# Kernel tuning notes

Hardware: AMD Instinct MI355X
Metric: run time of the kernel (lower is better)

Reference implementation:

```python
import jax, jax.numpy as jnp
import numpy as np

EMBED_DIM = 256
SEQ_LEN = 4096
BATCH = 8
ALPHA = 0.99


def setup_inputs() -> dict:
    key = jax.random.key(0)
    k_x, k_w, k_b = jax.random.split(key, 3)
    x = jax.random.normal(k_x, (BATCH, SEQ_LEN, EMBED_DIM), dtype=jnp.float32)
    # nn.Linear(embed_dim, 3*embed_dim): store as [d, 3d] so y = x @ Wqkv + bqkv
    Wqkv = jax.random.normal(k_w, (EMBED_DIM, 3 * EMBED_DIM), dtype=jnp.float32) * (EMBED_DIM ** -0.5)
    bqkv = jax.random.normal(k_b, (3 * EMBED_DIM,), dtype=jnp.float32) * 0.02
    return {"x": x, "Wqkv": Wqkv, "bqkv": bqkv}


def reference(x, Wqkv, bqkv):
    bs, sl, d = x.shape
    qkv = x @ Wqkv + bqkv                      # [bs, sl, 3d]
    q, k, v = jnp.split(qkv, 3, axis=-1)       # each [bs, sl, d]
    # causal * exponential-decay mask: M[i, j] = alpha**(i-j) for j <= i else 0
    i = jnp.arange(sl, dtype=jnp.float32)
    M = jnp.where(i[:, None] >= i[None, :],
                  jnp.power(jnp.float32(ALPHA), i[:, None] - i[None, :]),
                  0.0)                          # [sl, sl]
    scores = jnp.einsum('bqd,bkd->bqk', q, k) / jnp.sqrt(jnp.float32(d))
    out = jnp.einsum('bqk,bkd->bqd', scores * M, v)
    return out
```

## Files before the change

### kernel.cpp

```cpp
#include <hip/hip_runtime.h>

typedef __bf16 bf16x8 __attribute__((ext_vector_type(8)));
typedef float f32x4 __attribute__((ext_vector_type(4)));
typedef unsigned short u16;
typedef unsigned int u32;
typedef u16 u16x4 __attribute__((ext_vector_type(4)));

#define L2ALPHA (-0.014499569f)

static __device__ __forceinline__ u16 f2bf(float f) {
    u32 u = __builtin_bit_cast(u32, f);
    return (u16)((u + 0x7FFFu + ((u >> 16) & 1u)) >> 16);
}

static __device__ __forceinline__ void gl2lds16(const void* g, void* l) {
    __builtin_amdgcn_global_load_lds(
        (const __attribute__((address_space(1))) u32*)g,
        (__attribute__((address_space(3))) u32*)l, 16, 0, 0);
}

__global__ __launch_bounds__(256, 2) void proj_kernel(
        const float* __restrict__ x, const float* __restrict__ Wq,
        const float* __restrict__ bias,
        u16* __restrict__ qb, u16* __restrict__ kb, u16* __restrict__ vb)
{
    __shared__ __align__(16) u16 Bs[32 * 128 * 8];
    __shared__ __align__(16) u16 As[4 * 128 * 8];

    const int tid = threadIdx.x, lane = tid & 63, w = tid >> 6;
    const int l = blockIdx.x;
    const int nb = l >> 6;
    const int chunk = ((l >> 3) & 7) * 8 + (l & 7);
    const int n0 = nb * 128;
    const int wr = (w & 1) * 64, wc = (w >> 1) * 64;
    const int m = lane & 15, quad = lane >> 4;

    {
        const int col = tid & 127;
        const int khalf = tid >> 7;
        #pragma unroll
        for (int s = 0; s < 32; ++s) {
            int k0 = (khalf + 2 * s) * 4;
            u16x4 h;
            #pragma unroll
            for (int i = 0; i < 4; ++i)
                h[i] = f2bf(Wq[(k0 + i) * 768 + n0 + col]);
            *(u16x4*)&Bs[((k0 >> 3) * 128 + col) * 8 + (k0 & 7)] = h;
        }
    }

    for (int it = 0; it < 4; ++it) {
        const int m0 = (chunk * 4 + it) * 128;

        f32x4 acc[4][4];
        #pragma unroll
        for (int rt = 0; rt < 4; ++rt)
            #pragma unroll
            for (int ct = 0; ct < 4; ++ct)
                acc[rt][ct] = f32x4{0.f, 0.f, 0.f, 0.f};

        for (int kt = 0; kt < 8; ++kt) {
            __syncthreads();
            #pragma unroll
            for (int s = 0; s < 4; ++s) {
                int c = tid + 256 * s;
                int row = c >> 3, part = c & 7;
                const float4 v4 = *(const float4*)(x + (size_t)(m0 + row) * 256 + kt * 32 + part * 4);
                u16x4 h;
                h[0] = f2bf(v4.x); h[1] = f2bf(v4.y); h[2] = f2bf(v4.z); h[3] = f2bf(v4.w);
                *(u16x4*)&As[((part >> 1) * 128 + row) * 8 + (part & 1) * 4] = h;
            }
            __syncthreads();

            bf16x8 af[4], bfr[4];
            #pragma unroll
            for (int rt = 0; rt < 4; ++rt)
                af[rt] = *(const bf16x8*)&As[(quad * 128 + wr + rt * 16 + m) * 8];
            #pragma unroll
            for (int ct = 0; ct < 4; ++ct)
                bfr[ct] = *(const bf16x8*)&Bs[((kt * 4 + quad) * 128 + wc + ct * 16 + m) * 8];
            #pragma unroll
            for (int rt = 0; rt < 4; ++rt)
                #pragma unroll
                for (int ct = 0; ct < 4; ++ct)
                    acc[rt][ct] = __builtin_amdgcn_mfma_f32_16x16x32_bf16(
                        af[rt], bfr[ct], acc[rt][ct], 0, 0, 0);
        }

        const int b = m0 >> 12;
        const int jbase = (m0 & 4095) + wr;
        const int d0 = (nb & 1) * 128;

        if (nb < 2) {
            #pragma unroll
            for (int rt = 0; rt < 4; ++rt)
                #pragma unroll
                for (int ct = 0; ct < 4; ++ct) {
                    int coll = wc + ct * 16 + m;
                    float bv = bias[d0 + coll];
                    #pragma unroll
                    for (int r = 0; r < 4; ++r) {
                        int row = m0 + wr + rt * 16 + quad * 4 + r;
                        qb[(size_t)row * 256 + d0 + coll] = f2bf((acc[rt][ct][r] + bv) * 0.0625f);
                    }
                }
        } else if (nb < 4) {
            #pragma unroll
            for (int rt = 0; rt < 4; ++rt)
                #pragma unroll
                for (int ct = 0; ct < 4; ++ct) {
                    int d = d0 + wc + ct * 16 + m;
                    float bv = bias[256 + d];
                    int k8 = d >> 5, qk = (d >> 3) & 3, e = d & 7;
                    #pragma unroll
                    for (int r = 0; r < 4; ++r) {
                        int j = jbase + rt * 16 + quad * 4 + r;
                        int jt = j >> 5, hh = (j >> 4) & 1, mk = j & 15;
                        kb[((((size_t)(b * 128 + jt) * 2 + hh) * 8 + k8) * 64 + qk * 16 + mk) * 8 + e]
                            = f2bf(acc[rt][ct][r] + bv);
                    }
                }
        } else {
            #pragma unroll
            for (int rt = 0; rt < 4; ++rt)
                #pragma unroll
                for (int ct = 0; ct < 4; ++ct) {
                    int d = d0 + wc + ct * 16 + m;
                    float bv = bias[512 + d];
                    int dt = d >> 4, mv = d & 15;
                    int j = jbase + rt * 16 + quad * 4;
                    int jt = j >> 5, qv = (j >> 3) & 3, e0 = j & 7;
                    u16x4 hv;
                    #pragma unroll
                    for (int r = 0; r < 4; ++r) hv[r] = f2bf(acc[rt][ct][r] + bv);
                    *(u16x4*)&vb[(((size_t)(b * 128 + jt) * 16 + dt) * 64 + qv * 16 + mv) * 8 + e0] = hv;
                }
        }
    }
}

__global__ __launch_bounds__(256, 1) void attn_kernel(
        const u16* __restrict__ qb, const u16* __restrict__ kb,
        const u16* __restrict__ vb, float* __restrict__ out)
{
    __shared__ __align__(16) u16 Kf[2][8192];
    __shared__ __align__(16) u16 Vf[2][8192];
    __shared__ __align__(16) u16 Ps[4 * 2 * 16 * 40];

    const int tid = threadIdx.x, lane = tid & 63, w = tid >> 6;
    const int l = blockIdx.x;
    const int b = l & 7;
    const int m0 = (l >> 3) * 128;
    const int qrow0 = m0 + w * 32;
    const int m = lane & 15, quad = lane >> 4;
    const size_t rowbase = (size_t)b * 4096;

    bf16x8 qf[2][8];
    #pragma unroll
    for (int rg = 0; rg < 2; ++rg)
        #pragma unroll
        for (int k8 = 0; k8 < 8; ++k8)
            qf[rg][k8] = *(const bf16x8*)(qb + (rowbase + qrow0 + rg * 16 + m) * 256 + k8 * 32 + quad * 8);

    f32x4 acc[2][16];
    #pragma unroll
    for (int rg = 0; rg < 2; ++rg)
        #pragma unroll
        for (int dt = 0; dt < 16; ++dt)
            acc[rg][dt] = f32x4{0.f, 0.f, 0.f, 0.f};

    int t0 = (m0 - 1024) >> 5; if (t0 < 0) t0 = 0;
    const int t1 = (m0 >> 5) + 3;

    {
        const u16* kp = kb + (size_t)(b * 128 + t0) * 8192;
        const u16* vp = vb + (size_t)(b * 128 + t0) * 8192;
        #pragma unroll
        for (int s = 0; s < 4; ++s) {
            int c = tid + 256 * s;
            gl2lds16(kp + (size_t)c * 8, &Kf[0][c * 8]);
            gl2lds16(vp + (size_t)c * 8, &Vf[0][c * 8]);
        }
    }

    int p = 0;
    for (int t = t0; t <= t1; ++t) {
        __syncthreads();
        if (t < t1) {
            const u16* kp = kb + (size_t)(b * 128 + t + 1) * 8192;
            const u16* vp = vb + (size_t)(b * 128 + t + 1) * 8192;
            #pragma unroll
            for (int s = 0; s < 4; ++s) {
                int c = tid + 256 * s;
                gl2lds16(kp + (size_t)c * 8, &Kf[p ^ 1][c * 8]);
                gl2lds16(vp + (size_t)c * 8, &Vf[p ^ 1][c * 8]);
            }
        }
        const int j0 = t * 32;

        f32x4 s00{0.f,0.f,0.f,0.f}, s01{0.f,0.f,0.f,0.f};
        f32x4 s10{0.f,0.f,0.f,0.f}, s11{0.f,0.f,0.f,0.f};
        #pragma unroll
        for (int k8 = 0; k8 < 8; ++k8) {
            bf16x8 bf0 = *(const bf16x8*)&Kf[p][(k8 * 64 + lane) * 8];
            s00 = __builtin_amdgcn_mfma_f32_16x16x32_bf16(qf[0][k8], bf0, s00, 0, 0, 0);
            s01 = __builtin_amdgcn_mfma_f32_16x16x32_bf16(qf[1][k8], bf0, s01, 0, 0, 0);
        }
        #pragma unroll
        for (int k8 = 0; k8 < 8; ++k8) {
            bf16x8 bf1 = *(const bf16x8*)&Kf[p][((8 + k8) * 64 + lane) * 8];
            s10 = __builtin_amdgcn_mfma_f32_16x16x32_bf16(qf[0][k8], bf1, s10, 0, 0, 0);
            s11 = __builtin_amdgcn_mfma_f32_16x16x32_bf16(qf[1][k8], bf1, s11, 0, 0, 0);
        }

        #pragma unroll
        for (int rg = 0; rg < 2; ++rg) {
            f32x4 sh0 = rg ? s01 : s00;
            f32x4 sh1 = rg ? s11 : s10;
            #pragma unroll
            for (int r = 0; r < 4; ++r) {
                int i = qrow0 + rg * 16 + quad * 4 + r;
                int dd0 = i - (j0 + m);
                int dd1 = dd0 - 16;
                float w0 = (dd0 >= 0) ? __builtin_amdgcn_exp2f((float)dd0 * L2ALPHA) : 0.0f;
                float w1 = (dd1 >= 0) ? __builtin_amdgcn_exp2f((float)dd1 * L2ALPHA) : 0.0f;
                int rowb = ((w * 2 + rg) * 16 + quad * 4 + r) * 40;
                Ps[rowb + m]      = f2bf(sh0[r] * w0);
                Ps[rowb + 16 + m] = f2bf(sh1[r] * w1);
            }
        }
        asm volatile("s_waitcnt lgkmcnt(0)" ::: "memory");

        bf16x8 pa0 = *(const bf16x8*)&Ps[((w * 2 + 0) * 16 + m) * 40 + quad * 8];
        bf16x8 pa1 = *(const bf16x8*)&Ps[((w * 2 + 1) * 16 + m) * 40 + quad * 8];

        #pragma unroll
        for (int dt = 0; dt < 16; ++dt) {
            bf16x8 vf = *(const bf16x8*)&Vf[p][(dt * 64 + lane) * 8];
            acc[0][dt] = __builtin_amdgcn_mfma_f32_16x16x32_bf16(pa0, vf, acc[0][dt], 0, 0, 0);
            acc[1][dt] = __builtin_amdgcn_mfma_f32_16x16x32_bf16(pa1, vf, acc[1][dt], 0, 0, 0);
        }
        p ^= 1;
    }

    #pragma unroll
    for (int rg = 0; rg < 2; ++rg)
        #pragma unroll
        for (int dt = 0; dt < 16; ++dt)
            #pragma unroll
            for (int r = 0; r < 4; ++r)
                out[(rowbase + qrow0 + rg * 16 + quad * 4 + r) * 256 + dt * 16 + m] = acc[rg][dt][r];
}

extern "C" void kernel_launch(void* const* d_in, const int* in_sizes, int n_in,
                              void* d_out, int out_size, void* d_ws, size_t ws_size,
                              hipStream_t stream) {
    (void)in_sizes; (void)n_in; (void)out_size; (void)ws_size;
    const float* x    = (const float*)d_in[0];
    const float* Wq   = (const float*)d_in[1];
    const float* bias = (const float*)d_in[2];
    float* outp = (float*)d_out;

    const size_t per = (size_t)8 * 4096 * 256;
    u16* qb = (u16*)d_ws;
    u16* kb = qb + per;
    u16* vb = kb + per;

    proj_kernel<<<384, 256, 0, stream>>>(x, Wq, bias, qb, kb, vb);
    attn_kernel<<<256, 256, 0, stream>>>(qb, kb, vb, outp);
}
```

Baseline: 208.5 us.

## Use 8 waves of 16 query rows per attention block and skip out-of-window tiles

Doubles the attention block to 512 threads, so each of 8 waves owns 16 query rows instead of 4 waves owning 32. This halves per-wave registers and accumulators and raises the number of waves resident per CU. Each wave also skips the QK and PV MFMAs for key tiles outside its causal/truncated window, which cuts wasted work at the window edges. The tradeoff is that each loaded K/V fragment now feeds half as many MFMAs per LDS read, which lowers reuse of LDS reads.

```diff
diff --git a/kernel.cpp b/kernel.cpp
--- a/kernel.cpp
+++ b/kernel.cpp
@@ -139,35 +139,30 @@
     }
 }
 
-__global__ __launch_bounds__(256, 1) void attn_kernel(
+__global__ __launch_bounds__(512, 2) void attn_kernel(
         const u16* __restrict__ qb, const u16* __restrict__ kb,
         const u16* __restrict__ vb, float* __restrict__ out)
 {
     __shared__ __align__(16) u16 Kf[2][8192];
     __shared__ __align__(16) u16 Vf[2][8192];
-    __shared__ __align__(16) u16 Ps[4 * 2 * 16 * 40];
+    __shared__ __align__(16) u16 Ps[8 * 16 * 40];
 
     const int tid = threadIdx.x, lane = tid & 63, w = tid >> 6;
     const int l = blockIdx.x;
     const int b = l & 7;
     const int m0 = (l >> 3) * 128;
-    const int qrow0 = m0 + w * 32;
+    const int qrow0 = m0 + w * 16;
     const int m = lane & 15, quad = lane >> 4;
     const size_t rowbase = (size_t)b * 4096;
 
-    bf16x8 qf[2][8];
+    bf16x8 qf[8];
     #pragma unroll
-    for (int rg = 0; rg < 2; ++rg)
-        #pragma unroll
-        for (int k8 = 0; k8 < 8; ++k8)
-            qf[rg][k8] = *(const bf16x8*)(qb + (rowbase + qrow0 + rg * 16 + m) * 256 + k8 * 32 + quad * 8);
-
-    f32x4 acc[2][16];
+    for (int k8 = 0; k8 < 8; ++k8)
+        qf[k8] = *(const bf16x8*)(qb + (rowbase + qrow0 + m) * 256 + k8 * 32 + quad * 8);
+
+    f32x4 acc[16];
     #pragma unroll
-    for (int rg = 0; rg < 2; ++rg)
-        #pragma unroll
-        for (int dt = 0; dt < 16; ++dt)
-            acc[rg][dt] = f32x4{0.f, 0.f, 0.f, 0.f};
+    for (int dt = 0; dt < 16; ++dt) acc[dt] = f32x4{0.f, 0.f, 0.f, 0.f};
 
     int t0 = (m0 - 1024) >> 5; if (t0 < 0) t0 = 0;
     const int t1 = (m0 >> 5) + 3;
@@ -176,8 +171,8 @@
         const u16* kp = kb + (size_t)(b * 128 + t0) * 8192;
         const u16* vp = vb + (size_t)(b * 128 + t0) * 8192;
         #pragma unroll
-        for (int s = 0; s < 4; ++s) {
-            int c = tid + 256 * s;
+        for (int s = 0; s < 2; ++s) {
+            int c = tid + 512 * s;
             gl2lds16(kp + (size_t)c * 8, &Kf[0][c * 8]);
             gl2lds16(vp + (size_t)c * 8, &Vf[0][c * 8]);
         }
@@ -190,66 +185,56 @@
             const u16* kp = kb + (size_t)(b * 128 + t + 1) * 8192;
             const u16* vp = vb + (size_t)(b * 128 + t + 1) * 8192;
             #pragma unroll
-            for (int s = 0; s < 4; ++s) {
-                int c = tid + 256 * s;
+            for (int s = 0; s < 2; ++s) {
+                int c = tid + 512 * s;
                 gl2lds16(kp + (size_t)c * 8, &Kf[p ^ 1][c * 8]);
                 gl2lds16(vp + (size_t)c * 8, &Vf[p ^ 1][c * 8]);
             }
         }
         const int j0 = t * 32;
 
-        f32x4 s00{0.f,0.f,0.f,0.f}, s01{0.f,0.f,0.f,0.f};
-        f32x4 s10{0.f,0.f,0.f,0.f}, s11{0.f,0.f,0.f,0.f};
-        #pragma unroll
-        for (int k8 = 0; k8 < 8; ++k8) {
-            bf16x8 bf0 = *(const bf16x8*)&Kf[p][(k8 * 64 + lane) * 8];
-            s00 = __builtin_amdgcn_mfma_f32_16x16x32_bf16(qf[0][k8], bf0, s00, 0, 0, 0);
-            s01 = __builtin_amdgcn_mfma_f32_16x16x32_bf16(qf[1][k8], bf0, s01, 0, 0, 0);
-        }
-        #pragma unroll
-        for (int k8 = 0; k8 < 8; ++k8) {
-            bf16x8 bf1 = *(const bf16x8*)&Kf[p][((8 + k8) * 64 + lane) * 8];
-            s10 = __builtin_amdgcn_mfma_f32_16x16x32_bf16(qf[0][k8], bf1, s10, 0, 0, 0);
-            s11 = __builtin_amdgcn_mfma_f32_16x16x32_bf16(qf[1][k8], bf1, s11, 0, 0, 0);
-        }
-
-        #pragma unroll
-        for (int rg = 0; rg < 2; ++rg) {
-            f32x4 sh0 = rg ? s01 : s00;
-            f32x4 sh1 = rg ? s11 : s10;
+        if (j0 <= qrow0 + 15 && j0 + 1055 >= qrow0) {
+            f32x4 s0{0.f,0.f,0.f,0.f}, s1{0.f,0.f,0.f,0.f};
+            #pragma unroll
+            for (int k8 = 0; k8 < 8; ++k8) {
+                bf16x8 bf0 = *(const bf16x8*)&Kf[p][(k8 * 64 + lane) * 8];
+                s0 = __builtin_amdgcn_mfma_f32_16x16x32_bf16(qf[k8], bf0, s0, 0, 0, 0);
+            }
+            #pragma unroll
+            for (int k8 = 0; k8 < 8; ++k8) {
+                bf16x8 bf1 = *(const bf16x8*)&Kf[p][((8 + k8) * 64 + lane) * 8];
+                s1 = __builtin_amdgcn_mfma_f32_16x16x32_bf16(qf[k8], bf1, s1, 0, 0, 0);
+            }
+
             #pragma unroll
             for (int r = 0; r < 4; ++r) {
-                int i = qrow0 + rg * 16 + quad * 4 + r;
+                int i = qrow0 + quad * 4 + r;
                 int dd0 = i - (j0 + m);
                 int dd1 = dd0 - 16;
                 float w0 = (dd0 >= 0) ? __builtin_amdgcn_exp2f((float)dd0 * L2ALPHA) : 0.0f;
                 float w1 = (dd1 >= 0) ? __builtin_amdgcn_exp2f((float)dd1 * L2ALPHA) : 0.0f;
-                int rowb = ((w * 2 + rg) * 16 + quad * 4 + r) * 40;
-                Ps[rowb + m]      = f2bf(sh0[r] * w0);
-                Ps[rowb + 16 + m] = f2bf(sh1[r] * w1);
-            }
-        }
-        asm volatile("s_waitcnt lgkmcnt(0)" ::: "memory");
-
-        bf16x8 pa0 = *(const bf16x8*)&Ps[((w * 2 + 0) * 16 + m) * 40 + quad * 8];
-        bf16x8 pa1 = *(const bf16x8*)&Ps[((w * 2 + 1) * 16 + m) * 40 + quad * 8];
-
-        #pragma unroll
-        for (int dt = 0; dt < 16; ++dt) {
-            bf16x8 vf = *(const bf16x8*)&Vf[p][(dt * 64 + lane) * 8];
-            acc[0][dt] = __builtin_amdgcn_mfma_f32_16x16x32_bf16(pa0, vf, acc[0][dt], 0, 0, 0);
-            acc[1][dt] = __builtin_amdgcn_mfma_f32_16x16x32_bf16(pa1, vf, acc[1][dt], 0, 0, 0);
+                int rowb = (w * 16 + quad * 4 + r) * 40;
+                Ps[rowb + m]      = f2bf(s0[r] * w0);
+                Ps[rowb + 16 + m] = f2bf(s1[r] * w1);
+            }
+            asm volatile("s_waitcnt lgkmcnt(0)" ::: "memory");
+
+            bf16x8 pa = *(const bf16x8*)&Ps[(w * 16 + m) * 40 + quad * 8];
+
+            #pragma unroll
+            for (int dt = 0; dt < 16; ++dt) {
+                bf16x8 vf = *(const bf16x8*)&Vf[p][(dt * 64 + lane) * 8];
+                acc[dt] = __builtin_amdgcn_mfma_f32_16x16x32_bf16(pa, vf, acc[dt], 0, 0, 0);
+            }
         }
         p ^= 1;
     }
 
     #pragma unroll
-    for (int rg = 0; rg < 2; ++rg)
-        #pragma unroll
-        for (int dt = 0; dt < 16; ++dt)
-            #pragma unroll
-            for (int r = 0; r < 4; ++r)
-                out[(rowbase + qrow0 + rg * 16 + quad * 4 + r) * 256 + dt * 16 + m] = acc[rg][dt][r];
+    for (int dt = 0; dt < 16; ++dt)
+        #pragma unroll
+        for (int r = 0; r < 4; ++r)
+            out[(rowbase + qrow0 + quad * 4 + r) * 256 + dt * 16 + m] = acc[dt][r];
 }
 
 extern "C" void kernel_launch(void* const* d_in, const int* in_sizes, int n_in,
@@ -267,5 +252,5 @@
     u16* vb = kb + per;
 
     proj_kernel<<<384, 256, 0, stream>>>(x, Wq, bias, qb, kb, vb);
-    attn_kernel<<<256, 256, 0, stream>>>(qb, kb, vb, outp);
-}
+    attn_kernel<<<256, 512, 0, stream>>>(qb, kb, vb, outp);
+}
```

Measured after the change: 191.1 us. -8.3%, faster.

## Split projection into per-tile blocks with wave-private staging; skip out-of-window attention tiles

Applied to the files above, without the earlier changes.

The projection kernel now launches one block per 128x128 output tile instead of looping over four tiles. Each wave converts its own 32 rows of x into a private LDS slab, with register prefetch of the next k-slice, so the per-k-step block-wide barriers are gone. The cost is that every block reloads and converts the full W column slab, which is more repeated weight traffic. The attention kernel raises its launch bound to two blocks per CU and lets each wave skip the QK/PV work for key tiles that fall outside its causal and decay window.

```diff
diff --git a/kernel.cpp b/kernel.cpp
--- a/kernel.cpp
+++ b/kernel.cpp
@@ -5,6 +5,7 @@
 typedef unsigned short u16;
 typedef unsigned int u32;
 typedef u16 u16x4 __attribute__((ext_vector_type(4)));
+typedef u16 u16x8 __attribute__((ext_vector_type(8)));
 
 #define L2ALPHA (-0.014499569f)
 
@@ -25,14 +26,13 @@
         u16* __restrict__ qb, u16* __restrict__ kb, u16* __restrict__ vb)
 {
     __shared__ __align__(16) u16 Bs[32 * 128 * 8];
-    __shared__ __align__(16) u16 As[4 * 128 * 8];
+    __shared__ __align__(16) u16 As[4][32 * 40];
 
     const int tid = threadIdx.x, lane = tid & 63, w = tid >> 6;
     const int l = blockIdx.x;
-    const int nb = l >> 6;
-    const int chunk = ((l >> 3) & 7) * 8 + (l & 7);
-    const int n0 = nb * 128;
-    const int wr = (w & 1) * 64, wc = (w >> 1) * 64;
+    const int nb = l % 6;
+    const int mt = l / 6;
+    const int m0 = mt * 128, n0 = nb * 128;
     const int m = lane & 15, quad = lane >> 4;
 
     {
@@ -48,104 +48,116 @@
             *(u16x4*)&Bs[((k0 >> 3) * 128 + col) * 8 + (k0 & 7)] = h;
         }
     }
-
-    for (int it = 0; it < 4; ++it) {
-        const int m0 = (chunk * 4 + it) * 128;
-
-        f32x4 acc[4][4];
-        #pragma unroll
-        for (int rt = 0; rt < 4; ++rt)
-            #pragma unroll
-            for (int ct = 0; ct < 4; ++ct)
-                acc[rt][ct] = f32x4{0.f, 0.f, 0.f, 0.f};
-
-        for (int kt = 0; kt < 8; ++kt) {
-            __syncthreads();
-            #pragma unroll
-            for (int s = 0; s < 4; ++s) {
-                int c = tid + 256 * s;
-                int row = c >> 3, part = c & 7;
-                const float4 v4 = *(const float4*)(x + (size_t)(m0 + row) * 256 + kt * 32 + part * 4);
-                u16x4 h;
-                h[0] = f2bf(v4.x); h[1] = f2bf(v4.y); h[2] = f2bf(v4.z); h[3] = f2bf(v4.w);
-                *(u16x4*)&As[((part >> 1) * 128 + row) * 8 + (part & 1) * 4] = h;
-            }
-            __syncthreads();
-
-            bf16x8 af[4], bfr[4];
-            #pragma unroll
-            for (int rt = 0; rt < 4; ++rt)
-                af[rt] = *(const bf16x8*)&As[(quad * 128 + wr + rt * 16 + m) * 8];
-            #pragma unroll
-            for (int ct = 0; ct < 4; ++ct)
-                bfr[ct] = *(const bf16x8*)&Bs[((kt * 4 + quad) * 128 + wc + ct * 16 + m) * 8];
-            #pragma unroll
-            for (int rt = 0; rt < 4; ++rt)
-                #pragma unroll
-                for (int ct = 0; ct < 4; ++ct)
-                    acc[rt][ct] = __builtin_amdgcn_mfma_f32_16x16x32_bf16(
-                        af[rt], bfr[ct], acc[rt][ct], 0, 0, 0);
-        }
-
-        const int b = m0 >> 12;
-        const int jbase = (m0 & 4095) + wr;
-        const int d0 = (nb & 1) * 128;
-
-        if (nb < 2) {
-            #pragma unroll
-            for (int rt = 0; rt < 4; ++rt)
-                #pragma unroll
-                for (int ct = 0; ct < 4; ++ct) {
-                    int coll = wc + ct * 16 + m;
-                    float bv = bias[d0 + coll];
-                    #pragma unroll
-                    for (int r = 0; r < 4; ++r) {
-                        int row = m0 + wr + rt * 16 + quad * 4 + r;
-                        qb[(size_t)row * 256 + d0 + coll] = f2bf((acc[rt][ct][r] + bv) * 0.0625f);
-                    }
+    __syncthreads();
+
+    const int r = lane & 31, h = lane >> 5;
+    const float* xrow = x + (size_t)(m0 + w * 32 + r) * 256 + h * 16;
+    u16* As_w = &As[w][0];
+
+    f32x4 acc[2][8];
+    #pragma unroll
+    for (int rt = 0; rt < 2; ++rt)
+        #pragma unroll
+        for (int ct = 0; ct < 8; ++ct)
+            acc[rt][ct] = f32x4{0.f, 0.f, 0.f, 0.f};
+
+    float4 g0 = *(const float4*)(xrow + 0);
+    float4 g1 = *(const float4*)(xrow + 4);
+    float4 g2 = *(const float4*)(xrow + 8);
+    float4 g3 = *(const float4*)(xrow + 12);
+
+    for (int kt = 0; kt < 8; ++kt) {
+        u16x8 ha, hb;
+        ha[0]=f2bf(g0.x); ha[1]=f2bf(g0.y); ha[2]=f2bf(g0.z); ha[3]=f2bf(g0.w);
+        ha[4]=f2bf(g1.x); ha[5]=f2bf(g1.y); ha[6]=f2bf(g1.z); ha[7]=f2bf(g1.w);
+        hb[0]=f2bf(g2.x); hb[1]=f2bf(g2.y); hb[2]=f2bf(g2.z); hb[3]=f2bf(g2.w);
+        hb[4]=f2bf(g3.x); hb[5]=f2bf(g3.y); hb[6]=f2bf(g3.z); hb[7]=f2bf(g3.w);
+        *(u16x8*)&As_w[r * 40 + h * 16]     = ha;
+        *(u16x8*)&As_w[r * 40 + h * 16 + 8] = hb;
+
+        if (kt < 7) {
+            const float* xn = xrow + (kt + 1) * 32;
+            g0 = *(const float4*)(xn + 0);
+            g1 = *(const float4*)(xn + 4);
+            g2 = *(const float4*)(xn + 8);
+            g3 = *(const float4*)(xn + 12);
+        }
+
+        asm volatile("s_waitcnt lgkmcnt(0)" ::: "memory");
+
+        bf16x8 af[2], bfr[8];
+        #pragma unroll
+        for (int rt = 0; rt < 2; ++rt)
+            af[rt] = *(const bf16x8*)&As_w[(rt * 16 + m) * 40 + quad * 8];
+        #pragma unroll
+        for (int ct = 0; ct < 8; ++ct)
+            bfr[ct] = *(const bf16x8*)&Bs[((kt * 4 + quad) * 128 + ct * 16 + m) * 8];
+        #pragma unroll
+        for (int rt = 0; rt < 2; ++rt)
+            #pragma unroll
+            for (int ct = 0; ct < 8; ++ct)
+                acc[rt][ct] = __builtin_amdgcn_mfma_f32_16x16x32_bf16(
+                    af[rt], bfr[ct], acc[rt][ct], 0, 0, 0);
+    }
+
+    const int b = m0 >> 12;
+    const int jbase = (m0 & 4095) + w * 32;
+    const int d0 = (nb & 1) * 128;
+
+    if (nb < 2) {
+        #pragma unroll
+        for (int rt = 0; rt < 2; ++rt)
+            #pragma unroll
+            for (int ct = 0; ct < 8; ++ct) {
+                int coll = ct * 16 + m;
+                float bv = bias[d0 + coll];
+                #pragma unroll
+                for (int rr = 0; rr < 4; ++rr) {
+                    int row = m0 + w * 32 + rt * 16 + quad * 4 + rr;
+                    qb[(size_t)row * 256 + d0 + coll] = f2bf((acc[rt][ct][rr] + bv) * 0.0625f);
                 }
-        } else if (nb < 4) {
-            #pragma unroll
-            for (int rt = 0; rt < 4; ++rt)
-                #pragma unroll
-                for (int ct = 0; ct < 4; ++ct) {
-                    int d = d0 + wc + ct * 16 + m;
-                    float bv = bias[256 + d];
-                    int k8 = d >> 5, qk = (d >> 3) & 3, e = d & 7;
-                    #pragma unroll
-                    for (int r = 0; r < 4; ++r) {
-                        int j = jbase + rt * 16 + quad * 4 + r;
-                        int jt = j >> 5, hh = (j >> 4) & 1, mk = j & 15;
-                        kb[((((size_t)(b * 128 + jt) * 2 + hh) * 8 + k8) * 64 + qk * 16 + mk) * 8 + e]
-                            = f2bf(acc[rt][ct][r] + bv);
-                    }
+            }
+    } else if (nb < 4) {
+        #pragma unroll
+        for (int rt = 0; rt < 2; ++rt)
+            #pragma unroll
+            for (int ct = 0; ct < 8; ++ct) {
+                int d = d0 + ct * 16 + m;
+                float bv = bias[256 + d];
+                int k8 = d >> 5, qk = (d >> 3) & 3, e = d & 7;
+                #pragma unroll
+                for (int rr = 0; rr < 4; ++rr) {
+                    int j = jbase + rt * 16 + quad * 4 + rr;
+                    int jt = j >> 5, hh = (j >> 4) & 1, mk = j & 15;
+                    kb[((((size_t)(b * 128 + jt) * 2 + hh) * 8 + k8) * 64 + qk * 16 + mk) * 8 + e]
+                        = f2bf(acc[rt][ct][rr] + bv);
                 }
-        } else {
-            #pragma unroll
-            for (int rt = 0; rt < 4; ++rt)
-                #pragma unroll
-                for (int ct = 0; ct < 4; ++ct) {
-                    int d = d0 + wc + ct * 16 + m;
-                    float bv = bias[512 + d];
-                    int dt = d >> 4, mv = d & 15;
-                    int j = jbase + rt * 16 + quad * 4;
-                    int jt = j >> 5, qv = (j >> 3) & 3, e0 = j & 7;
-                    u16x4 hv;
-                    #pragma unroll
-                    for (int r = 0; r < 4; ++r) hv[r] = f2bf(acc[rt][ct][r] + bv);
-                    *(u16x4*)&vb[(((size_t)(b * 128 + jt) * 16 + dt) * 64 + qv * 16 + mv) * 8 + e0] = hv;
-                }
-        }
-    }
-}
-
-__global__ __launch_bounds__(256, 1) void attn_kernel(
+            }
+    } else {
+        #pragma unroll
+        for (int rt = 0; rt < 2; ++rt)
+            #pragma unroll
+            for (int ct = 0; ct < 8; ++ct) {
+                int d = d0 + ct * 16 + m;
+                float bv = bias[512 + d];
+                int dt = d >> 4, mv = d & 15;
+                int j = jbase + rt * 16 + quad * 4;
+                int jt = j >> 5, qv = (j >> 3) & 3, e0 = j & 7;
+                u16x4 hv;
+                #pragma unroll
+                for (int rr = 0; rr < 4; ++rr) hv[rr] = f2bf(acc[rt][ct][rr] + bv);
+                *(u16x4*)&vb[(((size_t)(b * 128 + jt) * 16 + dt) * 64 + qv * 16 + mv) * 8 + e0] = hv;
+            }
+    }
+}
+
+__global__ __launch_bounds__(256, 2) void attn_kernel(
         const u16* __restrict__ qb, const u16* __restrict__ kb,
         const u16* __restrict__ vb, float* __restrict__ out)
 {
     __shared__ __align__(16) u16 Kf[2][8192];
     __shared__ __align__(16) u16 Vf[2][8192];
-    __shared__ __align__(16) u16 Ps[4 * 2 * 16 * 40];
+    __shared__ __align__(16) u16 Ps[4 * 32 * 40];
 
     const int tid = threadIdx.x, lane = tid & 63, w = tid >> 6;
     const int l = blockIdx.x;
@@ -198,47 +210,49 @@
         }
         const int j0 = t * 32;
 
-        f32x4 s00{0.f,0.f,0.f,0.f}, s01{0.f,0.f,0.f,0.f};
-        f32x4 s10{0.f,0.f,0.f,0.f}, s11{0.f,0.f,0.f,0.f};
-        #pragma unroll
-        for (int k8 = 0; k8 < 8; ++k8) {
-            bf16x8 bf0 = *(const bf16x8*)&Kf[p][(k8 * 64 + lane) * 8];
-            s00 = __builtin_amdgcn_mfma_f32_16x16x32_bf16(qf[0][k8], bf0, s00, 0, 0, 0);
-            s01 = __builtin_amdgcn_mfma_f32_16x16x32_bf16(qf[1][k8], bf0, s01, 0, 0, 0);
-        }
-        #pragma unroll
-        for (int k8 = 0; k8 < 8; ++k8) {
-            bf16x8 bf1 = *(const bf16x8*)&Kf[p][((8 + k8) * 64 + lane) * 8];
-            s10 = __builtin_amdgcn_mfma_f32_16x16x32_bf16(qf[0][k8], bf1, s10, 0, 0, 0);
-            s11 = __builtin_amdgcn_mfma_f32_16x16x32_bf16(qf[1][k8], bf1, s11, 0, 0, 0);
-        }
-
-        #pragma unroll
-        for (int rg = 0; rg < 2; ++rg) {
-            f32x4 sh0 = rg ? s01 : s00;
-            f32x4 sh1 = rg ? s11 : s10;
-            #pragma unroll
-            for (int r = 0; r < 4; ++r) {
-                int i = qrow0 + rg * 16 + quad * 4 + r;
-                int dd0 = i - (j0 + m);
-                int dd1 = dd0 - 16;
-                float w0 = (dd0 >= 0) ? __builtin_amdgcn_exp2f((float)dd0 * L2ALPHA) : 0.0f;
-                float w1 = (dd1 >= 0) ? __builtin_amdgcn_exp2f((float)dd1 * L2ALPHA) : 0.0f;
-                int rowb = ((w * 2 + rg) * 16 + quad * 4 + r) * 40;
-                Ps[rowb + m]      = f2bf(sh0[r] * w0);
-                Ps[rowb + 16 + m] = f2bf(sh1[r] * w1);
-            }
-        }
-        asm volatile("s_waitcnt lgkmcnt(0)" ::: "memory");
-
-        bf16x8 pa0 = *(const bf16x8*)&Ps[((w * 2 + 0) * 16 + m) * 40 + quad * 8];
-        bf16x8 pa1 = *(const bf16x8*)&Ps[((w * 2 + 1) * 16 + m) * 40 + quad * 8];
-
-        #pragma unroll
-        for (int dt = 0; dt < 16; ++dt) {
-            bf16x8 vf = *(const bf16x8*)&Vf[p][(dt * 64 + lane) * 8];
-            acc[0][dt] = __builtin_amdgcn_mfma_f32_16x16x32_bf16(pa0, vf, acc[0][dt], 0, 0, 0);
-            acc[1][dt] = __builtin_amdgcn_mfma_f32_16x16x32_bf16(pa1, vf, acc[1][dt], 0, 0, 0);
+        if (j0 <= qrow0 + 31 && j0 + 1055 >= qrow0) {
+            f32x4 sA0{0.f,0.f,0.f,0.f}, sA1{0.f,0.f,0.f,0.f};
+            f32x4 sB0{0.f,0.f,0.f,0.f}, sB1{0.f,0.f,0.f,0.f};
+            #pragma unroll
+            for (int k8 = 0; k8 < 8; ++k8) {
+                bf16x8 bf0 = *(const bf16x8*)&Kf[p][(k8 * 64 + lane) * 8];
+                sA0 = __builtin_amdgcn_mfma_f32_16x16x32_bf16(qf[0][k8], bf0, sA0, 0, 0, 0);
+                sA1 = __builtin_amdgcn_mfma_f32_16x16x32_bf16(qf[1][k8], bf0, sA1, 0, 0, 0);
+            }
+            #pragma unroll
+            for (int k8 = 0; k8 < 8; ++k8) {
+                bf16x8 bf1 = *(const bf16x8*)&Kf[p][((8 + k8) * 64 + lane) * 8];
+                sB0 = __builtin_amdgcn_mfma_f32_16x16x32_bf16(qf[0][k8], bf1, sB0, 0, 0, 0);
+                sB1 = __builtin_amdgcn_mfma_f32_16x16x32_bf16(qf[1][k8], bf1, sB1, 0, 0, 0);
+            }
+
+            #pragma unroll
+            for (int rg = 0; rg < 2; ++rg) {
+                f32x4 sh0 = rg ? sA1 : sA0;
+                f32x4 sh1 = rg ? sB1 : sB0;
+                #pragma unroll
+                for (int rr = 0; rr < 4; ++rr) {
+                    int i = qrow0 + rg * 16 + quad * 4 + rr;
+                    int dd0 = i - (j0 + m);
+                    int dd1 = dd0 - 16;
+                    float w0 = (dd0 >= 0) ? __builtin_amdgcn_exp2f((float)dd0 * L2ALPHA) : 0.0f;
+                    float w1 = (dd1 >= 0) ? __builtin_amdgcn_exp2f((float)dd1 * L2ALPHA) : 0.0f;
+                    int rowb = (w * 32 + rg * 16 + quad * 4 + rr) * 40;
+                    Ps[rowb + m]      = f2bf(sh0[rr] * w0);
+                    Ps[rowb + 16 + m] = f2bf(sh1[rr] * w1);
+                }
+            }
+            asm volatile("s_waitcnt lgkmcnt(0)" ::: "memory");
+
+            bf16x8 pa0 = *(const bf16x8*)&Ps[(w * 32 + m) * 40 + quad * 8];
+            bf16x8 pa1 = *(const bf16x8*)&Ps[(w * 32 + 16 + m) * 40 + quad * 8];
+
+            #pragma unroll
+            for (int dt = 0; dt < 16; ++dt) {
+                bf16x8 vf = *(const bf16x8*)&Vf[p][(dt * 64 + lane) * 8];
+                acc[0][dt] = __builtin_amdgcn_mfma_f32_16x16x32_bf16(pa0, vf, acc[0][dt], 0, 0, 0);
+                acc[1][dt] = __builtin_amdgcn_mfma_f32_16x16x32_bf16(pa1, vf, acc[1][dt], 0, 0, 0);
+            }
         }
         p ^= 1;
     }
@@ -248,8 +262,8 @@
         #pragma unroll
         for (int dt = 0; dt < 16; ++dt)
             #pragma unroll
-            for (int r = 0; r < 4; ++r)
-                out[(rowbase + qrow0 + rg * 16 + quad * 4 + r) * 256 + dt * 16 + m] = acc[rg][dt][r];
+            for (int rr = 0; rr < 4; ++rr)
+                out[(rowbase + qrow0 + rg * 16 + quad * 4 + rr) * 256 + dt * 16 + m] = acc[rg][dt][rr];
 }
 
 extern "C" void kernel_launch(void* const* d_in, const int* in_sizes, int n_in,
@@ -266,6 +280,6 @@
     u16* kb = qb + per;
     u16* vb = kb + per;
 
-    proj_kernel<<<384, 256, 0, stream>>>(x, Wq, bias, qb, kb, vb);
+    proj_kernel<<<1536, 256, 0, stream>>>(x, Wq, bias, qb, kb, vb);
     attn_kernel<<<256, 256, 0, stream>>>(qb, kb, vb, outp);
 }
```

Result: faster. 197.0 us (-5.5%).
